# Optimization experiments

Measured on AMD Instinct MI355X. Metric: run time of the kernel, lower is better.

Reference implementation:

```python
import jax, jax.numpy as jnp
import numpy as np

EPS = 0.001
WEIGHT = 1.0


def _grid_sample_zeros(x, grid):
    """Bilinear grid_sample, align_corners=True, zeros padding.
    x: [B,C,H,W], grid: [B,H,W,2] in [-1,1] (x then y). Returns [B,C,H,W]."""
    B, C, H, W = x.shape
    gx = (grid[..., 0] + 1.0) * 0.5 * (W - 1)  # [B,H,W] pixel coords
    gy = (grid[..., 1] + 1.0) * 0.5 * (H - 1)
    x0 = jnp.floor(gx)
    y0 = jnp.floor(gy)
    x1 = x0 + 1.0
    y1 = y0 + 1.0
    wx1 = gx - x0
    wx0 = 1.0 - wx1
    wy1 = gy - y0
    wy0 = 1.0 - wy1

    def corner(xi, yi, w):
        valid = ((xi >= 0) & (xi <= W - 1) & (yi >= 0) & (yi <= H - 1)).astype(x.dtype)
        xc = jnp.clip(xi.astype(jnp.int32), 0, W - 1)
        yc = jnp.clip(yi.astype(jnp.int32), 0, H - 1)
        vals = jax.vmap(lambda img, yy, xx: img[:, yy, xx])(x, yc, xc)  # [B,C,H,W]
        return vals * (w * valid)[:, None, :, :]

    return (corner(x0, y0, wx0 * wy0) + corner(x1, y0, wx1 * wy0)
            + corner(x0, y1, wx0 * wy1) + corner(x1, y1, wx1 * wy1))


def _warp(x, flo):
    """Warp x by flow flo (pixel units), with validity mask. x,flo: [B,*,H,W]."""
    B, C, H, W = x.shape
    xx = jnp.arange(W, dtype=x.dtype)[None, :]  # [1,W]
    yy = jnp.arange(H, dtype=x.dtype)[:, None]  # [H,1]
    grid = jnp.stack([jnp.broadcast_to(xx, (H, W)), jnp.broadcast_to(yy, (H, W))], 0)  # [2,H,W]
    vgrid = grid[None] + flo  # [B,2,H,W]
    vx = 2.0 * vgrid[:, 0] / max(W - 1, 1) - 1.0
    vy = 2.0 * vgrid[:, 1] / max(H - 1, 1) - 1.0
    vgrid_n = jnp.stack([vx, vy], -1)  # [B,H,W,2]
    out = _grid_sample_zeros(x, vgrid_n)
    ones = jnp.ones_like(x)
    mask = _grid_sample_zeros(ones, vgrid_n)
    mask = jnp.where(mask < 0.9999, 0.0, 1.0).astype(x.dtype)
    mask = jax.lax.stop_gradient(mask)  # torch writes constants in-place -> no grad
    return out * mask


def setup_inputs() -> dict:
    key = jax.random.key(0)
    k1, k2 = jax.random.split(key)
    N, H, W = 16, 768, 768
    UV_AtoB = jax.random.normal(k1, (N, 2, H, W), dtype=jnp.float32)
    UV_BtoA = jax.random.normal(k2, (N, 2, H, W), dtype=jnp.float32)
    return {"UV_AtoB": UV_AtoB, "UV_BtoA": UV_BtoA}


def reference(UV_AtoB, UV_BtoA):
    N, C, H, W = UV_AtoB.shape
    xx = jnp.broadcast_to(jnp.arange(W, dtype=jnp.float32)[None, :], (H, W))
    yy = jnp.broadcast_to(jnp.arange(H, dtype=jnp.float32)[:, None], (H, W))
    GridXY = jnp.stack([xx / max(W - 1, 1), yy / max(H - 1, 1)], 0)  # [2,H,W]
    GridXY = jnp.broadcast_to(GridXY[None], (N, 2, H, W))

    def cycle_loss(flo1, flo2):
        m = _warp(GridXY, flo1)
        m = _warp(m, flo2)
        diff = jnp.sqrt(jnp.sum((GridXY - m) ** 2, axis=1) + EPS ** 2)  # [N,H,W]
        per = jnp.sum(diff, axis=(1, 2)) / (H * W)
        return jnp.sum(per) / N

    totloss_ABA = cycle_loss(UV_AtoB, UV_BtoA)
    totloss_BAB = cycle_loss(UV_BtoA, UV_AtoB)
    return (totloss_BAB + totloss_ABA) * WEIGHT
```

## Files before the change

kernel.cpp:

```cpp
#include <hip/hip_runtime.h>

constexpr int N = 16, H = 768, W = 768;
constexpr int HW = H * W;
constexpr float EPS2 = 1.0e-6f;
constexpr float INV = 1.0f / 767.0f;
constexpr float WM1 = 767.0f, WM2 = 766.0f, HM1 = 767.0f;
constexpr float CHALF  = 383.5f;
constexpr float CHALFI = 383.0f;

constexpr int TILE_COLS = 80;
constexpr int TILE_ROWS = 24;
constexpr int C_HALO = 8;
constexpr int R_HALO = 4;
constexpr int LSTRIDE = TILE_COLS;
constexpr int TILE_FLOATS = TILE_ROWS * LSTRIDE * 2;
constexpr int NBLK_X = W / 64, NBLK_Y = H / 16;
constexpr int NBLOCKS = NBLK_X * NBLK_Y * N;

typedef float v2f __attribute__((ext_vector_type(2)));
typedef float float2a __attribute__((ext_vector_type(2), aligned(4)));

struct DirMeta { v2f g; v2f f0; int xb, y0, y1; };

__device__ __forceinline__ void dir_meta(v2f flow, v2f xy, DirMeta& m) {
    m.g = xy + flow;
    m.f0 = (v2f){floorf(m.g.x), floorf(m.g.y)};
    m.xb = (int)fminf(fmaxf(m.f0.x, 0.0f), WM2);
    m.y0 = (int)fminf(fmaxf(m.f0.y, 0.0f), HM1);
    m.y1 = (int)fminf(fmaxf(m.f0.y + 1.0f, 0.0f), HM1);
}

__device__ __forceinline__ bool fast_ok(v2f f0, v2f u0, v2f v0, v2f u1, v2f v1) {
    v2f c  = f0 - CHALF;
    v2f c1 = c + 1.0f;
    v2f d00 = c  + u0;
    v2f d11 = c1 + v1;
    float d01x = c1.x + v0.x, d01y = c.y  + v0.y;
    float d10x = c.x  + u1.x, d10y = c1.y + u1.y;
    float xm = fmaxf(fabsf(d00.x), fabsf(d01x));
    xm = fmaxf(xm, fmaxf(fabsf(d10x), fabsf(d11.x)));
    float ym = fmaxf(fabsf(d00.y), fabsf(d01y));
    ym = fmaxf(ym, fmaxf(fabsf(d10y), fabsf(d11.y)));
    v2f t = c + 0.5f;
    return (xm <= CHALF) & (ym <= CHALF)
         & (fabsf(t.x) <= CHALFI) & (fabsf(t.y) <= CHALFI);
}

__device__ __forceinline__ float fast_eval(const DirMeta& m,
                                           v2f u0, v2f v0, v2f u1, v2f v1,
                                           v2f cen) {
    v2f w = m.g - m.f0;
    v2f wx = (v2f){w.x, w.x};
    v2f wy = (v2f){w.y, w.y};
    v2f ft = u0 + wx * (v0 - u0);
    v2f fb = u1 + wx * (v1 - u1);
    v2f fv = ft + wy * (fb - ft);
    v2f r = (cen + fv) * INV;
    return sqrtf(fmaf(r.x, r.x, fmaf(r.y, r.y, EPS2)));
}

__device__ __forceinline__ float2 wg(float fx, float fy, float xi, float yi) {
    float gx = xi + fx, gy = yi + fy;
    float x0 = floorf(gx), y0 = floorf(gy);
    float wx1 = gx - x0, wx0 = 1.0f - wx1;
    float wy1 = gy - y0, wy0 = 1.0f - wy1;
    float vx0 = (x0 >= 0.0f  && x0 <= WM1)        ? 1.0f : 0.0f;
    float vx1 = (x0 >= -1.0f && x0 <= WM1 - 1.0f) ? 1.0f : 0.0f;
    float vy0 = (y0 >= 0.0f  && y0 <= HM1)        ? 1.0f : 0.0f;
    float vy1 = (y0 >= -1.0f && y0 <= HM1 - 1.0f) ? 1.0f : 0.0f;
    float ax = wx0 * vx0, bx = wx1 * vx1, sx = ax + bx;
    float ay = wy0 * vy0, by = wy1 * vy1, sy = ay + by;
    float ms = sx * sy;
    float kx = (ms >= 0.9999f) ? INV : 0.0f;
    float ky = (ms >= 0.9999f) ? INV : 0.0f;
    float2 r;
    r.x = fmaf(sx, x0, bx) * sy * kx;
    r.y = fmaf(sy, y0, by) * sx * ky;
    return r;
}

__device__ __forceinline__ float dir_eval(const DirMeta& m,
                                          v2f u0, v2f v0, v2f u1, v2f v1,
                                          float xf, float yf) {
    float x0f = m.f0.x, y0f = m.f0.y;
    float wx1 = m.g.x - x0f, wx0 = 1.0f - wx1;
    float wy1 = m.g.y - y0f, wy0 = 1.0f - wy1;
    float x1f = x0f + 1.0f, y1f = y0f + 1.0f;
    float vx0 = (x0f >= 0.0f && x0f <= WM1) ? 1.0f : 0.0f;
    float vx1 = (x1f >= 0.0f && x1f <= WM1) ? 1.0f : 0.0f;
    float vy0 = (y0f >= 0.0f && y0f <= HM1) ? 1.0f : 0.0f;
    float vy1 = (y1f >= 0.0f && y1f <= HM1) ? 1.0f : 0.0f;
    float axw = wx0 * vx0, bxw = wx1 * vx1;
    float ayw = wy0 * vy0, byw = wy1 * vy1;
    float sxw = axw + bxw, syw = ayw + byw;
    float msum = sxw * syw;

    bool selA = (x0f >= WM1);
    bool selB = (x0f >= 0.0f);
    float fx00 = selA ? v0.x : u0.x;
    float fx01 = selB ? v0.x : u0.x;
    float fy00 = selA ? v0.y : u0.y;
    float fy01 = selB ? v0.y : u0.y;
    float fx10 = selA ? v1.x : u1.x;
    float fx11 = selB ? v1.x : u1.x;
    float fy10 = selA ? v1.y : u1.y;
    float fy11 = selB ? v1.y : u1.y;

    float x0c = fminf(fmaxf(x0f, 0.0f), WM1);
    float x1c = fminf(fmaxf(x1f, 0.0f), WM1);
    float y0c = fminf(fmaxf(y0f, 0.0f), HM1);
    float y1c = fminf(fmaxf(y1f, 0.0f), HM1);

    float2 m00 = wg(fx00, fy00, x0c, y0c);
    float2 m01 = wg(fx01, fy01, x1c, y0c);
    float2 m10 = wg(fx10, fy10, x0c, y1c);
    float2 m11 = wg(fx11, fy11, x1c, y1c);

    float w00 = axw * ayw, w10 = bxw * ayw, w01 = axw * byw, w11 = bxw * byw;
    float mx = w00 * m00.x + w10 * m01.x + w01 * m10.x + w11 * m11.x;
    float my = w00 * m00.y + w10 * m01.y + w01 * m10.y + w11 * m11.y;
    float keep = (msum >= 0.9999f) ? 1.0f : 0.0f;
    mx *= keep; my *= keep;

    float dx = xf * INV - mx;
    float dy = yf * INV - my;
    return sqrtf(fmaf(dx, dx, fmaf(dy, dy, EPS2)));
}

__device__ __forceinline__ void ld_quad(const float* t, int pix, v2f& u, v2f& v) {
    u = *(const v2f*)(t + 2 * pix);
    v = *(const v2f*)(t + 2 * pix + 2);
}

__global__ __launch_bounds__(256)
void cycle_loss_kernel(const float* __restrict__ A,
                       const float* __restrict__ B,
                       float* __restrict__ ws,
                       float* __restrict__ out,
                       int use_ws) {
    __shared__ float lds[2 * TILE_FLOATS];
    __shared__ float wsum[4];

    int tid  = threadIdx.x;
    int lane = tid & 63;
    int wv   = tid >> 6;
    int bx0 = blockIdx.x * 64;
    int by0 = blockIdx.y * 16;
    int b   = blockIdx.z;
    const float* Ab = A + (size_t)b * 2 * HW;
    const float* Bb = B + (size_t)b * 2 * HW;
    int tc0 = bx0 - C_HALO;
    int tr0 = by0 - R_HALO;

    constexpr int ROW_CHUNKS = TILE_COLS / 4;
    constexpr int TASKS_PER_T = TILE_ROWS * ROW_CHUNKS;
    for (int i = tid; i < 2 * TASKS_PER_T; i += 256) {
        int t   = i / TASKS_PER_T;
        int rem = i - t * TASKS_PER_T;
        int lr  = rem / ROW_CHUNKS;
        int lc4 = rem - lr * ROW_CHUNKS;
        int rg = tr0 + lr;
        int cg = tc0 + lc4 * 4;
        if ((unsigned)rg < (unsigned)H && (unsigned)cg < (unsigned)W) {
            const float* src = (t ? Bb : Ab) + rg * W + cg;
            float4 fx = *(const float4*)(src);
            float4 fy = *(const float4*)(src + HW);
            float* dst = &lds[t * TILE_FLOATS + (lr * LSTRIDE + lc4 * 4) * 2];
            *(float4*)(dst)     = make_float4(fx.x, fy.x, fx.y, fy.y);
            *(float4*)(dst + 4) = make_float4(fx.z, fy.z, fx.w, fy.w);
        }
    }
    __syncthreads();

    const float* ldsA = lds;
    const float* ldsB = lds + TILE_FLOATS;
    int x  = bx0 + lane;
    int yb = by0 + wv * 4;
    int lxc = lane + C_HALO;
    float xf = (float)x;

    v2f aC[4], bC[4];
    #pragma unroll
    for (int p = 0; p < 4; ++p) {
        int co = (wv * 4 + p + R_HALO) * LSTRIDE + lxc;
        aC[p] = *(const v2f*)(ldsA + 2 * co);
        bC[p] = *(const v2f*)(ldsB + 2 * co);
    }

    float s = 0.0f;
    #pragma unroll
    for (int p = 0; p < 4; ++p) {
        float yf = (float)(yb + p);
        v2f xy = (v2f){xf, yf};
        DirMeta m1, m2;
        dir_meta(bC[p], xy, m1);
        dir_meta(aC[p], xy, m2);

        int x1l = m1.xb - tc0, y1l0 = m1.y0 - tr0, y1l1 = m1.y1 - tr0;
        int x2l = m2.xb - tc0, y2l0 = m2.y0 - tr0, y2l1 = m2.y1 - tr0;
        bool e1 = ((unsigned)x1l <= (unsigned)(TILE_COLS - 2))
                & ((unsigned)y1l0 < (unsigned)TILE_ROWS)
                & ((unsigned)y1l1 < (unsigned)TILE_ROWS);
        bool e2 = ((unsigned)x2l <= (unsigned)(TILE_COLS - 2))
                & ((unsigned)y2l0 < (unsigned)TILE_ROWS)
                & ((unsigned)y2l1 < (unsigned)TILE_ROWS);

        v2f u10, v10, u11, v11, u20, v20, u21, v21;
        if (__all(e1 & e2)) {
            ld_quad(ldsA, y1l0 * LSTRIDE + x1l, u10, v10);
            ld_quad(ldsA, y1l1 * LSTRIDE + x1l, u11, v11);
            ld_quad(ldsB, y2l0 * LSTRIDE + x2l, u20, v20);
            ld_quad(ldsB, y2l1 * LSTRIDE + x2l, u21, v21);
        } else {
            if (e1) {
                ld_quad(ldsA, y1l0 * LSTRIDE + x1l, u10, v10);
                ld_quad(ldsA, y1l1 * LSTRIDE + x1l, u11, v11);
            } else {
                int o0 = m1.y0 * W + m1.xb, o1 = m1.y1 * W + m1.xb;
                float2a rx0 = *(const float2a*)(Ab + o0);
                float2a ry0 = *(const float2a*)(Ab + HW + o0);
                float2a rx1 = *(const float2a*)(Ab + o1);
                float2a ry1 = *(const float2a*)(Ab + HW + o1);
                u10 = (v2f){rx0.x, ry0.x}; v10 = (v2f){rx0.y, ry0.y};
                u11 = (v2f){rx1.x, ry1.x}; v11 = (v2f){rx1.y, ry1.y};
            }
            if (e2) {
                ld_quad(ldsB, y2l0 * LSTRIDE + x2l, u20, v20);
                ld_quad(ldsB, y2l1 * LSTRIDE + x2l, u21, v21);
            } else {
                int o0 = m2.y0 * W + m2.xb, o1 = m2.y1 * W + m2.xb;
                float2a rx0 = *(const float2a*)(Bb + o0);
                float2a ry0 = *(const float2a*)(Bb + HW + o0);
                float2a rx1 = *(const float2a*)(Bb + o1);
                float2a ry1 = *(const float2a*)(Bb + HW + o1);
                u20 = (v2f){rx0.x, ry0.x}; v20 = (v2f){rx0.y, ry0.y};
                u21 = (v2f){rx1.x, ry1.x}; v21 = (v2f){rx1.y, ry1.y};
            }
        }

        bool ok = fast_ok(m1.f0, u10, v10, u11, v11)
                & fast_ok(m2.f0, u20, v20, u21, v21);
        if (__all(ok)) {
            s += fast_eval(m1, u10, v10, u11, v11, bC[p]);
            s += fast_eval(m2, u20, v20, u21, v21, aC[p]);
        } else {
            s += dir_eval(m1, u10, v10, u11, v11, xf, yf);
            s += dir_eval(m2, u20, v20, u21, v21, xf, yf);
        }
    }

    #pragma unroll
    for (int o = 32; o > 0; o >>= 1) s += __shfl_down(s, o, 64);
    if (lane == 0) wsum[wv] = s;
    __syncthreads();
    if (tid == 0) {
        float tsum = wsum[0] + wsum[1] + wsum[2] + wsum[3];
        if (use_ws) {
            int bid = (blockIdx.z * gridDim.y + blockIdx.y) * gridDim.x + blockIdx.x;
            ws[bid] = tsum;
        } else {
            atomicAdd(out, tsum * (1.0f / ((float)N * (float)H * (float)W)));
        }
    }
}

__global__ __launch_bounds__(256)
void reduce_kernel(const float* __restrict__ ws, float* __restrict__ out) {
    float s = 0.0f;
    for (int i = threadIdx.x; i < NBLOCKS / 4; i += 256) {
        float4 v = *(const float4*)(ws + 4 * i);
        s += (v.x + v.y) + (v.z + v.w);
    }
    #pragma unroll
    for (int o = 32; o > 0; o >>= 1) s += __shfl_down(s, o, 64);
    __shared__ float wsum[4];
    int lane = threadIdx.x & 63, wv = threadIdx.x >> 6;
    if (lane == 0) wsum[wv] = s;
    __syncthreads();
    if (threadIdx.x == 0) {
        float t = wsum[0] + wsum[1] + wsum[2] + wsum[3];
        out[0] = t * (1.0f / ((float)N * (float)H * (float)W));
    }
}

extern "C" void kernel_launch(void* const* d_in, const int* in_sizes, int n_in,
                              void* d_out, int out_size, void* d_ws, size_t ws_size,
                              hipStream_t stream) {
    const float* A = (const float*)d_in[0];
    const float* B = (const float*)d_in[1];
    float* out = (float*)d_out;
    float* ws  = (float*)d_ws;

    int use_ws = (ws_size >= NBLOCKS * sizeof(float)) ? 1 : 0;
    if (!use_ws) hipMemsetAsync(out, 0, sizeof(float), stream);

    dim3 grid(NBLK_X, NBLK_Y, N);
    cycle_loss_kernel<<<grid, 256, 0, stream>>>(A, B, ws, out, use_ws);
    if (use_ws) reduce_kernel<<<1, 256, 0, stream>>>(ws, out);
}
```

Measured before the change: 201.3 us.

## Software-pipeline LDS gathers one row ahead and pad LDS stride

Restructures the per-pixel loop into a two-stage software pipeline. Each iteration issues the LDS gathers for row p unconditionally, using clamped addresses, while it runs the global fallback loads and the evaluation for row p-1. This is meant to hide LDS latency behind arithmetic and to remove the wave-wide __all branch around the gathers. The LDS row stride is padded from 80 to 84 to reduce bank conflicts, and launch bounds now request 4 blocks per CU. The trade-off is higher register pressure from holding two rows of gathered state, which could cause spills under the tighter occupancy bound.

```diff
diff --git a/kernel.cpp b/kernel.cpp
--- a/kernel.cpp
+++ b/kernel.cpp
@@ -12,22 +12,20 @@
 constexpr int TILE_ROWS = 24;
 constexpr int C_HALO = 8;
 constexpr int R_HALO = 4;
-constexpr int LSTRIDE = TILE_COLS;
+constexpr int LSTRIDE = 84;
 constexpr int TILE_FLOATS = TILE_ROWS * LSTRIDE * 2;
+constexpr int MAXPIX = TILE_ROWS * LSTRIDE - 2;
 constexpr int NBLK_X = W / 64, NBLK_Y = H / 16;
 constexpr int NBLOCKS = NBLK_X * NBLK_Y * N;
 
 typedef float v2f __attribute__((ext_vector_type(2)));
 typedef float float2a __attribute__((ext_vector_type(2), aligned(4)));
 
-struct DirMeta { v2f g; v2f f0; int xb, y0, y1; };
+struct DirMeta { v2f g; v2f f0; };
 
 __device__ __forceinline__ void dir_meta(v2f flow, v2f xy, DirMeta& m) {
     m.g = xy + flow;
     m.f0 = (v2f){floorf(m.g.x), floorf(m.g.y)};
-    m.xb = (int)fminf(fmaxf(m.f0.x, 0.0f), WM2);
-    m.y0 = (int)fminf(fmaxf(m.f0.y, 0.0f), HM1);
-    m.y1 = (int)fminf(fmaxf(m.f0.y + 1.0f, 0.0f), HM1);
 }
 
 __device__ __forceinline__ bool fast_ok(v2f f0, v2f u0, v2f v0, v2f u1, v2f v1) {
@@ -132,7 +130,43 @@
     v = *(const v2f*)(t + 2 * pix + 2);
 }
 
-__global__ __launch_bounds__(256)
+__device__ __forceinline__ void gather_issue(const float* tile, const DirMeta& m,
+                                             int tc0, int tr0, bool& e,
+                                             v2f& u0, v2f& v0, v2f& u1, v2f& v1) {
+    int xb = (int)fminf(fmaxf(m.f0.x, 0.0f), WM2);
+    int y0 = (int)fminf(fmaxf(m.f0.y, 0.0f), HM1);
+    int y1 = (int)fminf(fmaxf(m.f0.y + 1.0f, 0.0f), HM1);
+    int xl = xb - tc0, yl0 = y0 - tr0, yl1 = y1 - tr0;
+    e = ((unsigned)xl <= (unsigned)(TILE_COLS - 2))
+      & ((unsigned)yl0 < (unsigned)TILE_ROWS)
+      & ((unsigned)yl1 < (unsigned)TILE_ROWS);
+    unsigned p0 = min((unsigned)(yl0 * LSTRIDE + xl), (unsigned)MAXPIX);
+    unsigned p1 = min((unsigned)(yl1 * LSTRIDE + xl), (unsigned)MAXPIX);
+    ld_quad(tile, (int)p0, u0, v0);
+    ld_quad(tile, (int)p1, u1, v1);
+}
+
+__device__ __forceinline__ void gather_fallback(const float* base, const DirMeta& m,
+                                                v2f& u0, v2f& v0, v2f& u1, v2f& v1) {
+    int xb = (int)fminf(fmaxf(m.f0.x, 0.0f), WM2);
+    int y0 = (int)fminf(fmaxf(m.f0.y, 0.0f), HM1);
+    int y1 = (int)fminf(fmaxf(m.f0.y + 1.0f, 0.0f), HM1);
+    int o0 = y0 * W + xb, o1 = y1 * W + xb;
+    float2a rx0 = *(const float2a*)(base + o0);
+    float2a ry0 = *(const float2a*)(base + HW + o0);
+    float2a rx1 = *(const float2a*)(base + o1);
+    float2a ry1 = *(const float2a*)(base + HW + o1);
+    u0 = (v2f){rx0.x, ry0.x}; v0 = (v2f){rx0.y, ry0.y};
+    u1 = (v2f){rx1.x, ry1.x}; v1 = (v2f){rx1.y, ry1.y};
+}
+
+struct Pix {
+    DirMeta m1, m2;
+    bool e1, e2;
+    v2f u10, v10, u11, v11, u20, v20, u21, v21;
+};
+
+__global__ __launch_bounds__(256, 4)
 void cycle_loss_kernel(const float* __restrict__ A,
                        const float* __restrict__ B,
                        float* __restrict__ ws,
@@ -187,65 +221,39 @@
         bC[p] = *(const v2f*)(ldsB + 2 * co);
     }
 
+    Pix st[4];
     float s = 0.0f;
     #pragma unroll
-    for (int p = 0; p < 4; ++p) {
-        float yf = (float)(yb + p);
-        v2f xy = (v2f){xf, yf};
-        DirMeta m1, m2;
-        dir_meta(bC[p], xy, m1);
-        dir_meta(aC[p], xy, m2);
-
-        int x1l = m1.xb - tc0, y1l0 = m1.y0 - tr0, y1l1 = m1.y1 - tr0;
-        int x2l = m2.xb - tc0, y2l0 = m2.y0 - tr0, y2l1 = m2.y1 - tr0;
-        bool e1 = ((unsigned)x1l <= (unsigned)(TILE_COLS - 2))
-                & ((unsigned)y1l0 < (unsigned)TILE_ROWS)
-                & ((unsigned)y1l1 < (unsigned)TILE_ROWS);
-        bool e2 = ((unsigned)x2l <= (unsigned)(TILE_COLS - 2))
-                & ((unsigned)y2l0 < (unsigned)TILE_ROWS)
-                & ((unsigned)y2l1 < (unsigned)TILE_ROWS);
-
-        v2f u10, v10, u11, v11, u20, v20, u21, v21;
-        if (__all(e1 & e2)) {
-            ld_quad(ldsA, y1l0 * LSTRIDE + x1l, u10, v10);
-            ld_quad(ldsA, y1l1 * LSTRIDE + x1l, u11, v11);
-            ld_quad(ldsB, y2l0 * LSTRIDE + x2l, u20, v20);
-            ld_quad(ldsB, y2l1 * LSTRIDE + x2l, u21, v21);
-        } else {
-            if (e1) {
-                ld_quad(ldsA, y1l0 * LSTRIDE + x1l, u10, v10);
-                ld_quad(ldsA, y1l1 * LSTRIDE + x1l, u11, v11);
+    for (int q = 0; q < 5; ++q) {
+        if (q < 4) {
+            const int p = q;
+            float yf = (float)(yb + p);
+            v2f xy = (v2f){xf, yf};
+            dir_meta(bC[p], xy, st[p].m1);
+            dir_meta(aC[p], xy, st[p].m2);
+            gather_issue(ldsA, st[p].m1, tc0, tr0, st[p].e1,
+                         st[p].u10, st[p].v10, st[p].u11, st[p].v11);
+            gather_issue(ldsB, st[p].m2, tc0, tr0, st[p].e2,
+                         st[p].u20, st[p].v20, st[p].u21, st[p].v21);
+        }
+        if (q >= 1) {
+            const int p = q - 1;
+            float yf = (float)(yb + p);
+            if (!st[p].e1)
+                gather_fallback(Ab, st[p].m1,
+                                st[p].u10, st[p].v10, st[p].u11, st[p].v11);
+            if (!st[p].e2)
+                gather_fallback(Bb, st[p].m2,
+                                st[p].u20, st[p].v20, st[p].u21, st[p].v21);
+            bool ok = fast_ok(st[p].m1.f0, st[p].u10, st[p].v10, st[p].u11, st[p].v11)
+                    & fast_ok(st[p].m2.f0, st[p].u20, st[p].v20, st[p].u21, st[p].v21);
+            if (__all(ok)) {
+                s += fast_eval(st[p].m1, st[p].u10, st[p].v10, st[p].u11, st[p].v11, bC[p]);
+                s += fast_eval(st[p].m2, st[p].u20, st[p].v20, st[p].u21, st[p].v21, aC[p]);
             } else {
-                int o0 = m1.y0 * W + m1.xb, o1 = m1.y1 * W + m1.xb;
-                float2a rx0 = *(const float2a*)(Ab + o0);
-                float2a ry0 = *(const float2a*)(Ab + HW + o0);
-                float2a rx1 = *(const float2a*)(Ab + o1);
-                float2a ry1 = *(const float2a*)(Ab + HW + o1);
-                u10 = (v2f){rx0.x, ry0.x}; v10 = (v2f){rx0.y, ry0.y};
-                u11 = (v2f){rx1.x, ry1.x}; v11 = (v2f){rx1.y, ry1.y};
+                s += dir_eval(st[p].m1, st[p].u10, st[p].v10, st[p].u11, st[p].v11, xf, yf);
+                s += dir_eval(st[p].m2, st[p].u20, st[p].v20, st[p].u21, st[p].v21, xf, yf);
             }
-            if (e2) {
-                ld_quad(ldsB, y2l0 * LSTRIDE + x2l, u20, v20);
-                ld_quad(ldsB, y2l1 * LSTRIDE + x2l, u21, v21);
-            } else {
-                int o0 = m2.y0 * W + m2.xb, o1 = m2.y1 * W + m2.xb;
-                float2a rx0 = *(const float2a*)(Bb + o0);
-                float2a ry0 = *(const float2a*)(Bb + HW + o0);
-                float2a rx1 = *(const float2a*)(Bb + o1);
-                float2a ry1 = *(const float2a*)(Bb + HW + o1);
-                u20 = (v2f){rx0.x, ry0.x}; v20 = (v2f){rx0.y, ry0.y};
-                u21 = (v2f){rx1.x, ry1.x}; v21 = (v2f){rx1.y, ry1.y};
-            }
-        }
-
-        bool ok = fast_ok(m1.f0, u10, v10, u11, v11)
-                & fast_ok(m2.f0, u20, v20, u21, v21);
-        if (__all(ok)) {
-            s += fast_eval(m1, u10, v10, u11, v11, bC[p]);
-            s += fast_eval(m2, u20, v20, u21, v21, aC[p]);
-        } else {
-            s += dir_eval(m1, u10, v10, u11, v11, xf, yf);
-            s += dir_eval(m2, u20, v20, u21, v21, xf, yf);
         }
     }
 
```

New measurement: 220.7 us. 1.1x slower.

## Replace LDS tile staging with direct global gathers, one row per block

Applied to the files above, without the earlier changes.

Removes the shared-memory tile with halo and the cooperative staging loop and __syncthreads. Each block now handles one image row with 384 threads, each thread loading two adjacent pixels' flows directly and gathering bilinear neighbours from global memory through the cache. This drops the halo over-fetch, the LDS writes and the sync, but every gather now goes to L1/L2 instead of LDS, and the reduction workspace grows to one entry per row.

```diff
diff --git a/kernel.cpp b/kernel.cpp
--- a/kernel.cpp
+++ b/kernel.cpp
@@ -8,14 +8,8 @@
 constexpr float CHALF  = 383.5f;
 constexpr float CHALFI = 383.0f;
 
-constexpr int TILE_COLS = 80;
-constexpr int TILE_ROWS = 24;
-constexpr int C_HALO = 8;
-constexpr int R_HALO = 4;
-constexpr int LSTRIDE = TILE_COLS;
-constexpr int TILE_FLOATS = TILE_ROWS * LSTRIDE * 2;
-constexpr int NBLK_X = W / 64, NBLK_Y = H / 16;
-constexpr int NBLOCKS = NBLK_X * NBLK_Y * N;
+constexpr int NBLK_Y = H;
+constexpr int NBLOCKS = NBLK_Y * N;
 
 typedef float v2f __attribute__((ext_vector_type(2)));
 typedef float float2a __attribute__((ext_vector_type(2), aligned(4)));
@@ -28,6 +22,18 @@
     m.xb = (int)fminf(fmaxf(m.f0.x, 0.0f), WM2);
     m.y0 = (int)fminf(fmaxf(m.f0.y, 0.0f), HM1);
     m.y1 = (int)fminf(fmaxf(m.f0.y + 1.0f, 0.0f), HM1);
+}
+
+__device__ __forceinline__ void gather_global(const float* __restrict__ base,
+                                              const DirMeta& m,
+                                              v2f& u0, v2f& v0, v2f& u1, v2f& v1) {
+    int o0 = m.y0 * W + m.xb, o1 = m.y1 * W + m.xb;
+    float2a rx0 = *(const float2a*)(base + o0);
+    float2a ry0 = *(const float2a*)(base + HW + o0);
+    float2a rx1 = *(const float2a*)(base + o1);
+    float2a ry1 = *(const float2a*)(base + HW + o1);
+    u0 = (v2f){rx0.x, ry0.x}; v0 = (v2f){rx0.y, ry0.y};
+    u1 = (v2f){rx1.x, ry1.x}; v1 = (v2f){rx1.y, ry1.y};
 }
 
 __device__ __forceinline__ bool fast_ok(v2f f0, v2f u0, v2f v0, v2f u1, v2f v1) {
@@ -127,122 +133,51 @@
     return sqrtf(fmaf(dx, dx, fmaf(dy, dy, EPS2)));
 }
 
-__device__ __forceinline__ void ld_quad(const float* t, int pix, v2f& u, v2f& v) {
-    u = *(const v2f*)(t + 2 * pix);
-    v = *(const v2f*)(t + 2 * pix + 2);
-}
-
-__global__ __launch_bounds__(256)
+__global__ __launch_bounds__(384)
 void cycle_loss_kernel(const float* __restrict__ A,
                        const float* __restrict__ B,
                        float* __restrict__ ws,
                        float* __restrict__ out,
                        int use_ws) {
-    __shared__ float lds[2 * TILE_FLOATS];
-    __shared__ float wsum[4];
+    __shared__ float wsum[6];
 
     int tid  = threadIdx.x;
     int lane = tid & 63;
     int wv   = tid >> 6;
-    int bx0 = blockIdx.x * 64;
-    int by0 = blockIdx.y * 16;
-    int b   = blockIdx.z;
+    int y    = blockIdx.x;
+    int b    = blockIdx.y;
     const float* Ab = A + (size_t)b * 2 * HW;
     const float* Bb = B + (size_t)b * 2 * HW;
-    int tc0 = bx0 - C_HALO;
-    int tr0 = by0 - R_HALO;
-
-    constexpr int ROW_CHUNKS = TILE_COLS / 4;
-    constexpr int TASKS_PER_T = TILE_ROWS * ROW_CHUNKS;
-    for (int i = tid; i < 2 * TASKS_PER_T; i += 256) {
-        int t   = i / TASKS_PER_T;
-        int rem = i - t * TASKS_PER_T;
-        int lr  = rem / ROW_CHUNKS;
-        int lc4 = rem - lr * ROW_CHUNKS;
-        int rg = tr0 + lr;
-        int cg = tc0 + lc4 * 4;
-        if ((unsigned)rg < (unsigned)H && (unsigned)cg < (unsigned)W) {
-            const float* src = (t ? Bb : Ab) + rg * W + cg;
-            float4 fx = *(const float4*)(src);
-            float4 fy = *(const float4*)(src + HW);
-            float* dst = &lds[t * TILE_FLOATS + (lr * LSTRIDE + lc4 * 4) * 2];
-            *(float4*)(dst)     = make_float4(fx.x, fy.x, fx.y, fy.y);
-            *(float4*)(dst + 4) = make_float4(fx.z, fy.z, fx.w, fy.w);
-        }
-    }
-    __syncthreads();
-
-    const float* ldsA = lds;
-    const float* ldsB = lds + TILE_FLOATS;
-    int x  = bx0 + lane;
-    int yb = by0 + wv * 4;
-    int lxc = lane + C_HALO;
-    float xf = (float)x;
-
-    v2f aC[4], bC[4];
-    #pragma unroll
-    for (int p = 0; p < 4; ++p) {
-        int co = (wv * 4 + p + R_HALO) * LSTRIDE + lxc;
-        aC[p] = *(const v2f*)(ldsA + 2 * co);
-        bC[p] = *(const v2f*)(ldsB + 2 * co);
-    }
+
+    int x0 = tid * 2;
+    int rowoff = y * W + x0;
+    float2 aCx = *(const float2*)(Ab + rowoff);
+    float2 aCy = *(const float2*)(Ab + HW + rowoff);
+    float2 bCx = *(const float2*)(Bb + rowoff);
+    float2 bCy = *(const float2*)(Bb + HW + rowoff);
+    float yf = (float)y;
 
     float s = 0.0f;
     #pragma unroll
-    for (int p = 0; p < 4; ++p) {
-        float yf = (float)(yb + p);
+    for (int k = 0; k < 2; ++k) {
+        float xf = (float)(x0 + k);
+        v2f aC = (v2f){k ? aCx.y : aCx.x, k ? aCy.y : aCy.x};
+        v2f bC = (v2f){k ? bCx.y : bCx.x, k ? bCy.y : bCy.x};
         v2f xy = (v2f){xf, yf};
+
         DirMeta m1, m2;
-        dir_meta(bC[p], xy, m1);
-        dir_meta(aC[p], xy, m2);
-
-        int x1l = m1.xb - tc0, y1l0 = m1.y0 - tr0, y1l1 = m1.y1 - tr0;
-        int x2l = m2.xb - tc0, y2l0 = m2.y0 - tr0, y2l1 = m2.y1 - tr0;
-        bool e1 = ((unsigned)x1l <= (unsigned)(TILE_COLS - 2))
-                & ((unsigned)y1l0 < (unsigned)TILE_ROWS)
-                & ((unsigned)y1l1 < (unsigned)TILE_ROWS);
-        bool e2 = ((unsigned)x2l <= (unsigned)(TILE_COLS - 2))
-                & ((unsigned)y2l0 < (unsigned)TILE_ROWS)
-                & ((unsigned)y2l1 < (unsigned)TILE_ROWS);
+        dir_meta(bC, xy, m1);
+        dir_meta(aC, xy, m2);
 
         v2f u10, v10, u11, v11, u20, v20, u21, v21;
-        if (__all(e1 & e2)) {
-            ld_quad(ldsA, y1l0 * LSTRIDE + x1l, u10, v10);
-            ld_quad(ldsA, y1l1 * LSTRIDE + x1l, u11, v11);
-            ld_quad(ldsB, y2l0 * LSTRIDE + x2l, u20, v20);
-            ld_quad(ldsB, y2l1 * LSTRIDE + x2l, u21, v21);
-        } else {
-            if (e1) {
-                ld_quad(ldsA, y1l0 * LSTRIDE + x1l, u10, v10);
-                ld_quad(ldsA, y1l1 * LSTRIDE + x1l, u11, v11);
-            } else {
-                int o0 = m1.y0 * W + m1.xb, o1 = m1.y1 * W + m1.xb;
-                float2a rx0 = *(const float2a*)(Ab + o0);
-                float2a ry0 = *(const float2a*)(Ab + HW + o0);
-                float2a rx1 = *(const float2a*)(Ab + o1);
-                float2a ry1 = *(const float2a*)(Ab + HW + o1);
-                u10 = (v2f){rx0.x, ry0.x}; v10 = (v2f){rx0.y, ry0.y};
-                u11 = (v2f){rx1.x, ry1.x}; v11 = (v2f){rx1.y, ry1.y};
-            }
-            if (e2) {
-                ld_quad(ldsB, y2l0 * LSTRIDE + x2l, u20, v20);
-                ld_quad(ldsB, y2l1 * LSTRIDE + x2l, u21, v21);
-            } else {
-                int o0 = m2.y0 * W + m2.xb, o1 = m2.y1 * W + m2.xb;
-                float2a rx0 = *(const float2a*)(Bb + o0);
-                float2a ry0 = *(const float2a*)(Bb + HW + o0);
-                float2a rx1 = *(const float2a*)(Bb + o1);
-                float2a ry1 = *(const float2a*)(Bb + HW + o1);
-                u20 = (v2f){rx0.x, ry0.x}; v20 = (v2f){rx0.y, ry0.y};
-                u21 = (v2f){rx1.x, ry1.x}; v21 = (v2f){rx1.y, ry1.y};
-            }
-        }
+        gather_global(Ab, m1, u10, v10, u11, v11);
+        gather_global(Bb, m2, u20, v20, u21, v21);
 
         bool ok = fast_ok(m1.f0, u10, v10, u11, v11)
                 & fast_ok(m2.f0, u20, v20, u21, v21);
         if (__all(ok)) {
-            s += fast_eval(m1, u10, v10, u11, v11, bC[p]);
-            s += fast_eval(m2, u20, v20, u21, v21, aC[p]);
+            s += fast_eval(m1, u10, v10, u11, v11, bC);
+            s += fast_eval(m2, u20, v20, u21, v21, aC);
         } else {
             s += dir_eval(m1, u10, v10, u11, v11, xf, yf);
             s += dir_eval(m2, u20, v20, u21, v21, xf, yf);
@@ -254,9 +189,10 @@
     if (lane == 0) wsum[wv] = s;
     __syncthreads();
     if (tid == 0) {
-        float tsum = wsum[0] + wsum[1] + wsum[2] + wsum[3];
+        float tsum = ((wsum[0] + wsum[1]) + (wsum[2] + wsum[3]))
+                   + (wsum[4] + wsum[5]);
         if (use_ws) {
-            int bid = (blockIdx.z * gridDim.y + blockIdx.y) * gridDim.x + blockIdx.x;
+            int bid = blockIdx.y * gridDim.x + blockIdx.x;
             ws[bid] = tsum;
         } else {
             atomicAdd(out, tsum * (1.0f / ((float)N * (float)H * (float)W)));
@@ -294,7 +230,7 @@
     int use_ws = (ws_size >= NBLOCKS * sizeof(float)) ? 1 : 0;
     if (!use_ws) hipMemsetAsync(out, 0, sizeof(float), stream);
 
-    dim3 grid(NBLK_X, NBLK_Y, N);
-    cycle_loss_kernel<<<grid, 256, 0, stream>>>(A, B, ws, out, use_ws);
+    dim3 grid(NBLK_Y, N);
+    cycle_loss_kernel<<<grid, 384, 0, stream>>>(A, B, ws, out, use_ws);
     if (use_ws) reduce_kernel<<<1, 256, 0, stream>>>(ws, out);
 }
```

After: 263.5 us. 1.31x slower.
